# Optimization experiments

Measured on AMD Instinct MI355X. Metric: run time of the kernel, lower is better.

The kernel has to match this reference:

```python
import jax, jax.numpy as jnp
import numpy as np

N = 50000      # nodes
E = 400000     # edges per relation
R = 3          # edge types
D = 128        # input_dim == hidden_dim
H = 8          # attention heads
Dh = D // H    # per-head dim (16)
OUT = 1        # output logits
NEG_SLOPE = 0.2
LN_EPS = 1e-5


def setup_inputs() -> dict:
    key = jax.random.key(0)
    ks = jax.random.split(key, 20)
    s = 0.05
    f32 = jnp.float32
    return {
        "feat": jax.random.normal(ks[0], (N, D), f32),
        "edge_src": jax.random.randint(ks[1], (R, E), 0, N, dtype=jnp.int32),
        "edge_dst": jax.random.randint(ks[2], (R, E), 0, N, dtype=jnp.int32),
        # conv1: per-relation GATConv params (W, attn_l, attn_r, bias)
        "W1": jax.random.normal(ks[3], (R, D, H * Dh), f32) * s,
        "al1": jax.random.normal(ks[4], (R, H, Dh), f32) * s,
        "ar1": jax.random.normal(ks[5], (R, H, Dh), f32) * s,
        "b1": jnp.zeros((R, H * Dh), f32),
        # conv2
        "W2": jax.random.normal(ks[6], (R, D, H * Dh), f32) * s,
        "al2": jax.random.normal(ks[7], (R, H, Dh), f32) * s,
        "ar2": jax.random.normal(ks[8], (R, H, Dh), f32) * s,
        "b2": jnp.zeros((R, H * Dh), f32),
        # LayerNorm
        "ln_g": jnp.ones((D,), f32),
        "ln_b": jnp.zeros((D,), f32),
        # classifier MLP (dropout inactive at eval)
        "Wc1": jax.random.normal(ks[9], (D, D), f32) * s,
        "bc1": jnp.zeros((D,), f32),
        "Wc2": jax.random.normal(ks[10], (D, OUT), f32) * s,
        "bc2": jnp.zeros((OUT,), f32),
    }


def _gat(x, src, dst, W, al, ar, b):
    """DGL GATConv on one relation: x [N,Din] -> [N, H*Dh]."""
    h = (x @ W).reshape(N, H, Dh)                       # projected feats
    el = (h * al).sum(-1)                               # [N,H] src attn term
    er = (h * ar).sum(-1)                               # [N,H] dst attn term
    e = jax.nn.leaky_relu(el[src] + er[dst], NEG_SLOPE)  # [E,H]
    # edge-softmax over incoming edges per dst node, per head
    m = jax.ops.segment_max(e, dst, num_segments=N)     # [N,H]
    ex = jnp.exp(e - m[dst])
    denom = jax.ops.segment_sum(ex, dst, num_segments=N)
    alpha = ex / denom[dst]                             # [E,H]
    msg = alpha[:, :, None] * h[src]                    # [E,H,Dh]
    out = jax.ops.segment_sum(msg, dst, num_segments=N)  # [N,H,Dh]
    return out.reshape(N, H * Dh) + b


def _hetero(x, edge_src, edge_dst, W, al, ar, b):
    out = jnp.zeros((N, H * Dh), x.dtype)
    for r in range(R):  # small fixed relation count
        out = out + _gat(x, edge_src[r], edge_dst[r], W[r], al[r], ar[r], b[r])
    return out


def reference(feat, edge_src, edge_dst, W1, al1, ar1, b1, W2, al2, ar2, b2,
              ln_g, ln_b, Wc1, bc1, Wc2, bc2):
    h1 = jax.nn.relu(_hetero(feat, edge_src, edge_dst, W1, al1, ar1, b1))
    h2 = _hetero(h1, edge_src, edge_dst, W2, al2, ar2, b2)
    h = h2 + h1
    mu = h.mean(-1, keepdims=True)
    var = ((h - mu) ** 2).mean(-1, keepdims=True)
    h = (h - mu) * jax.lax.rsqrt(var + LN_EPS) * ln_g + ln_b
    h = jax.nn.relu(h @ Wc1 + bc1)
    return h @ Wc2 + bc2
```

## Files before the change

### kernel.cpp

```cpp
#include <hip/hip_runtime.h>
#include <math.h>

#define NN 50000
#define NE 400000
#define NREL 3
#define NCH 196

typedef __bf16 bf16x8 __attribute__((ext_vector_type(8)));
typedef float floatx4 __attribute__((ext_vector_type(4)));

__device__ __forceinline__ unsigned short f2bf(float f) {
  unsigned int u = __float_as_uint(f);
  return (unsigned short)((u + 0x7fffu + ((u >> 16) & 1u)) >> 16);
}

__global__ __launch_bounds__(256) void prep_wt(
    const float* __restrict__ W1, const float* __restrict__ W2,
    const float* __restrict__ Wc1, unsigned short* __restrict__ Wt) {
  int mat = blockIdx.x >> 3, slab = blockIdx.x & 7;
  const float* Wsrc = mat < 3 ? W1 + mat * 16384
                    : (mat < 6 ? W2 + (mat - 3) * 16384 : Wc1);
  unsigned short* dst = Wt + (size_t)mat * 144 * 128;
  int k0 = slab * 16;
#pragma unroll
  for (int i = 0; i < 8; ++i) {
    int idx = i * 256 + threadIdx.x;
    int k = k0 + (idx >> 7), nn = idx & 127;
    dst[nn * 128 + k] = f2bf(Wsrc[k * 128 + nn]);
  }
}

__global__ __launch_bounds__(256) void prep_attn(
    const float* __restrict__ W1, const float* __restrict__ W2,
    const float* __restrict__ al1, const float* __restrict__ ar1,
    const float* __restrict__ al2, const float* __restrict__ ar2,
    unsigned short* __restrict__ Wt) {
  int mat = blockIdx.x;
  const float* Wsrc = mat < 3 ? W1 + mat * 16384 : W2 + (mat - 3) * 16384;
  const float* alp = mat < 3 ? al1 + mat * 128 : al2 + (mat - 3) * 128;
  const float* arp = mat < 3 ? ar1 + mat * 128 : ar2 + (mat - 3) * 128;
  unsigned short* dst = Wt + (size_t)mat * 144 * 128;
#pragma unroll
  for (int i = 0; i < 8; ++i) {
    int j = i * 256 + threadIdx.x;
    int half = j >> 10, jj = j & 1023;
    int k = jj >> 3, h = jj & 7;
    const float* av = half ? arp : alp;
    float s = 0.f;
#pragma unroll
    for (int d = 0; d < 16; ++d) s += Wsrc[k * 128 + h * 16 + d] * av[h * 16 + d];
    dst[(128 + half * 8 + h) * 128 + k] = f2bf(s);
  }
}

__global__ __launch_bounds__(256) void gemm3_attn_mfma(
    const float* __restrict__ X, const unsigned short* __restrict__ Wt,
    unsigned short* __restrict__ hp, float* __restrict__ el,
    float* __restrict__ er, int n) {
  __shared__ unsigned short Xs[64 * 136];
  __shared__ unsigned short Ws[144 * 136];
  int t = threadIdx.x;
  int rowbase = blockIdx.x * 64;

  const float4* X4 = (const float4*)X;
#pragma unroll
  for (int i = 0; i < 8; ++i) {
    int v = t + i * 256;
    int row = v >> 5, k4 = (v & 31) * 4;
    float4 x = make_float4(0.f, 0.f, 0.f, 0.f);
    if (rowbase + row < n) x = X4[(size_t)(rowbase + row) * 32 + (v & 31)];
    ushort4 p;
    p.x = f2bf(x.x); p.y = f2bf(x.y); p.z = f2bf(x.z); p.w = f2bf(x.w);
    *(ushort4*)&Xs[row * 136 + k4] = p;
  }

  int lane = t & 63, wave = t >> 6;
  int quad = lane >> 4, l = lane & 15;

  for (int r = 0; r < NREL; ++r) {
    __syncthreads();
    const uint4* WtR = (const uint4*)(Wt + (size_t)r * 144 * 128);
#pragma unroll
    for (int i = 0; i < 9; ++i) {
      int v = t + i * 256;
      ((uint4*)Ws)[(v >> 4) * 17 + (v & 15)] = WtR[v];
    }
    __syncthreads();

    floatx4 acc[9];
#pragma unroll
    for (int i = 0; i < 9; ++i) acc[i] = floatx4{0.f, 0.f, 0.f, 0.f};
#pragma unroll
    for (int ks = 0; ks < 4; ++ks) {
      bf16x8 a = *(const bf16x8*)&Xs[(wave * 16 + l) * 136 + ks * 32 + quad * 8];
#pragma unroll
      for (int nt = 0; nt < 9; ++nt) {
        bf16x8 b = *(const bf16x8*)&Ws[(nt * 16 + l) * 136 + ks * 32 + quad * 8];
        acc[nt] = __builtin_amdgcn_mfma_f32_16x16x32_bf16(a, b, acc[nt], 0, 0, 0);
      }
    }

    unsigned short* hpR = hp + (size_t)r * NN * 128;
    float* elR = el + (size_t)r * NN * 8;
    float* erR = er + (size_t)r * NN * 8;
    int r0 = rowbase + wave * 16 + quad * 4;
#pragma unroll
    for (int reg = 0; reg < 4; ++reg) {
      int row = r0 + reg;
      if (row < n) {
#pragma unroll
        for (int nt = 0; nt < 8; ++nt)
          hpR[(size_t)row * 128 + nt * 16 + l] = f2bf(acc[nt][reg]);
        if (l < 8) elR[row * 8 + l] = acc[8][reg];
        else       erR[row * 8 + (l - 8)] = acc[8][reg];
      }
    }
  }
}

__global__ __launch_bounds__(256) void gemm_head_mfma(
    const float* __restrict__ X, const unsigned short* __restrict__ Wt,
    const float* __restrict__ bc1, const float* __restrict__ wc2,
    const float* __restrict__ bc2, float* __restrict__ out, int n) {
  __shared__ unsigned short Xs[64 * 136];
  __shared__ unsigned short Ws[128 * 136];
  int t = threadIdx.x;
  int rowbase = blockIdx.x * 64;

  const float4* X4 = (const float4*)X;
#pragma unroll
  for (int i = 0; i < 8; ++i) {
    int v = t + i * 256;
    int row = v >> 5, k4 = (v & 31) * 4;
    float4 x = make_float4(0.f, 0.f, 0.f, 0.f);
    if (rowbase + row < n) x = X4[(size_t)(rowbase + row) * 32 + (v & 31)];
    ushort4 p;
    p.x = f2bf(x.x); p.y = f2bf(x.y); p.z = f2bf(x.z); p.w = f2bf(x.w);
    *(ushort4*)&Xs[row * 136 + k4] = p;
  }
  const uint4* WtR = (const uint4*)Wt;
#pragma unroll
  for (int i = 0; i < 8; ++i) {
    int v = t + i * 256;
    ((uint4*)Ws)[(v >> 4) * 17 + (v & 15)] = WtR[v];
  }
  __syncthreads();

  int lane = t & 63, wave = t >> 6;
  int quad = lane >> 4, l = lane & 15;

  floatx4 acc[8];
#pragma unroll
  for (int i = 0; i < 8; ++i) acc[i] = floatx4{0.f, 0.f, 0.f, 0.f};
#pragma unroll
  for (int ks = 0; ks < 4; ++ks) {
    bf16x8 a = *(const bf16x8*)&Xs[(wave * 16 + l) * 136 + ks * 32 + quad * 8];
#pragma unroll
    for (int nt = 0; nt < 8; ++nt) {
      bf16x8 b = *(const bf16x8*)&Ws[(nt * 16 + l) * 136 + ks * 32 + quad * 8];
      acc[nt] = __builtin_amdgcn_mfma_f32_16x16x32_bf16(a, b, acc[nt], 0, 0, 0);
    }
  }

  float bv[8], wv[8];
#pragma unroll
  for (int nt = 0; nt < 8; ++nt) {
    bv[nt] = bc1[nt * 16 + l];
    wv[nt] = wc2[nt * 16 + l];
  }
  int r0 = rowbase + wave * 16 + quad * 4;
#pragma unroll
  for (int reg = 0; reg < 4; ++reg) {
    float s = 0.f;
#pragma unroll
    for (int nt = 0; nt < 8; ++nt)
      s += fmaxf(acc[nt][reg] + bv[nt], 0.f) * wv[nt];
    s += __shfl_xor(s, 1); s += __shfl_xor(s, 2);
    s += __shfl_xor(s, 4); s += __shfl_xor(s, 8);
    int row = r0 + reg;
    if (l == 0 && row < n) out[row] = s + bc2[0];
  }
}

__global__ __launch_bounds__(256) void hist_kernel(
    const int* __restrict__ edst, int* __restrict__ cnt, int* __restrict__ rank) {
  int t = blockIdx.x * 256 + threadIdx.x;
  if (t >= NREL * NE) return;
  int r = t / NE;
  rank[t] = atomicAdd(&cnt[r * NN + edst[t]], 1);
}

__global__ __launch_bounds__(256) void scan1(
    const int* __restrict__ cnt, int* __restrict__ partials) {
  __shared__ int s[256];
  int r = blockIdx.x / NCH, c = blockIdx.x % NCH;
  int i = c * 256 + threadIdx.x;
  s[threadIdx.x] = (i < NN) ? cnt[r * NN + i] : 0;
  __syncthreads();
  for (int off = 128; off; off >>= 1) {
    if (threadIdx.x < off) s[threadIdx.x] += s[threadIdx.x + off];
    __syncthreads();
  }
  if (threadIdx.x == 0) partials[r * NCH + c] = s[0];
}

__global__ __launch_bounds__(256) void scan2(int* __restrict__ partials) {
  __shared__ int s[256];
  int r = blockIdx.x;
  int t = threadIdx.x;
  int v = (t < NCH) ? partials[r * NCH + t] : 0;
  s[t] = v;
  __syncthreads();
  for (int off = 1; off < 256; off <<= 1) {
    int x = (t >= off) ? s[t - off] : 0;
    __syncthreads();
    s[t] += x;
    __syncthreads();
  }
  if (t < NCH) partials[r * NCH + t] = s[t] - v;
}

__global__ __launch_bounds__(256) void scan3(
    const int* __restrict__ cnt, const int* __restrict__ partials,
    int* __restrict__ rowptr) {
  __shared__ int s[256];
  int r = blockIdx.x / NCH, c = blockIdx.x % NCH;
  int t = threadIdx.x;
  int i = c * 256 + t;
  int v = (i < NN) ? cnt[r * NN + i] : 0;
  s[t] = v;
  __syncthreads();
  for (int off = 1; off < 256; off <<= 1) {
    int x = (t >= off) ? s[t - off] : 0;
    __syncthreads();
    s[t] += x;
    __syncthreads();
  }
  int base = partials[r * NCH + c];
  if (i < NN) rowptr[r * (NN + 1) + i] = base + s[t] - v;
  if (c == NCH - 1 && t == 0) rowptr[r * (NN + 1) + NN] = NE;
}

__global__ __launch_bounds__(256) void scatter_kernel(
    const int* __restrict__ esrc, const int* __restrict__ edst,
    const int* __restrict__ rowptr, const int* __restrict__ rank,
    int* __restrict__ col) {
  int t = blockIdx.x * 256 + threadIdx.x;
  if (t >= NREL * NE) return;
  int r = t / NE;
  int pos = rowptr[r * (NN + 1) + edst[t]] + rank[t];
  col[(size_t)r * NE + pos] = esrc[t];
}

__global__ __launch_bounds__(256) void gather_all(
    const int* __restrict__ rowptr, const int* __restrict__ col,
    const float* __restrict__ el, const float* __restrict__ er,
    const unsigned short* __restrict__ hp, const float* __restrict__ b,
    float* __restrict__ h1, const float* __restrict__ g,
    const float* __restrict__ beta, int mode) {
  int wid = (blockIdx.x * 256 + threadIdx.x) >> 6;
  int lane = threadIdx.x & 63;
  if (wid >= NN) return;
  int h = lane >> 3;
  int eoff = lane & 7;
  int c = lane * 2;

  int st3[NREL], en3[NREL], cv3[NREL];
  float er3[NREL];
#pragma unroll
  for (int r = 0; r < NREL; ++r) {
    const int* rp = rowptr + r * (NN + 1);
    st3[r] = rp[wid];
    en3[r] = rp[wid + 1];
    er3[r] = er[(size_t)r * NN * 8 + wid * 8 + h];
  }
#pragma unroll
  for (int r = 0; r < NREL; ++r) {
    int last = en3[r] - 1;
    last = last < st3[r] ? st3[r] : last;
    int i0 = st3[r] + eoff;
    cv3[r] = col[r * NE + (i0 < last ? i0 : last)];
  }

  float ax = 0.f, ay = 0.f;
#pragma unroll
  for (int r = 0; r < NREL; ++r) {
    int start = st3[r], end = en3[r];
    if (end > start) {
      const int* cl = col + r * NE;
      const float* elr = el + (size_t)r * NN * 8;
      const unsigned short* hpr = hp + (size_t)r * NN * 128;
      float er_me = er3[r];
      int last = end - 1;
      int idx = start + eoff;
      int colv = cv3[r];
      float den = 0.f, sx = 0.f, sy = 0.f;
      for (int i = start; i < end; i += 8) {
        int nidx = idx + 8;
        int colm = cl[nidx < last ? nidx : last];
        float e = elr[colv * 8 + h] + er_me;
        e = fmaxf(e, 0.2f * e);
        float x = (idx < end) ? __expf(e) : 0.f;
        den += x;
        unsigned int xi = __float_as_uint(x);
#define GATHER_EDGE(JJ)                                                        \
        {                                                                      \
          int sj = __builtin_amdgcn_readlane(colv, JJ);                        \
          const unsigned int* rowp = (const unsigned int*)(hpr + (size_t)sj * 128); \
          unsigned int u = rowp[lane];                                         \
          float xe = __uint_as_float(                                          \
              __builtin_amdgcn_ds_swizzle(xi, ((JJ) << 5) | 0x18));            \
          sx += xe * __uint_as_float(u << 16);                                 \
          sy += xe * __uint_as_float(u & 0xffff0000u);                         \
        }
        GATHER_EDGE(0)
        GATHER_EDGE(1)
        GATHER_EDGE(2)
        GATHER_EDGE(3)
        GATHER_EDGE(4)
        GATHER_EDGE(5)
        GATHER_EDGE(6)
        GATHER_EDGE(7)
#undef GATHER_EDGE
        idx = nidx;
        colv = colm;
      }
      den += __shfl_xor(den, 1);
      den += __shfl_xor(den, 2);
      den += __shfl_xor(den, 4);
      float inv = 1.f / den;
      ax += sx * inv;
      ay += sy * inv;
    }
  }

  float bx = b[c] + b[128 + c] + b[256 + c];
  float by = b[c + 1] + b[128 + c + 1] + b[256 + c + 1];
  float2* hptr = (float2*)&h1[(size_t)wid * 128 + c];
  if (mode == 0) {
    *hptr = make_float2(fmaxf(ax + bx, 0.f), fmaxf(ay + by, 0.f));
  } else {
    float2 r1 = *hptr;
    float vx = ax + bx + r1.x;
    float vy = ay + by + r1.y;
    float s = vx + vy;
#pragma unroll
    for (int off = 32; off; off >>= 1) s += __shfl_xor(s, off);
    float mu = s * (1.f / 128.f);
    float dx = vx - mu, dy = vy - mu;
    float sq = dx * dx + dy * dy;
#pragma unroll
    for (int off = 32; off; off >>= 1) sq += __shfl_xor(sq, off);
    float rstd = rsqrtf(sq * (1.f / 128.f) + 1e-5f);
    *hptr = make_float2(dx * rstd * g[c] + beta[c],
                        dy * rstd * g[c + 1] + beta[c + 1]);
  }
}

extern "C" void kernel_launch(void* const* d_in, const int* in_sizes, int n_in,
                              void* d_out, int out_size, void* d_ws, size_t ws_size,
                              hipStream_t stream) {
  const float* feat = (const float*)d_in[0];
  const int* esrc = (const int*)d_in[1];
  const int* edst = (const int*)d_in[2];
  const float* W1 = (const float*)d_in[3];
  const float* al1 = (const float*)d_in[4];
  const float* ar1 = (const float*)d_in[5];
  const float* b1 = (const float*)d_in[6];
  const float* W2 = (const float*)d_in[7];
  const float* al2 = (const float*)d_in[8];
  const float* ar2 = (const float*)d_in[9];
  const float* b2 = (const float*)d_in[10];
  const float* lng = (const float*)d_in[11];
  const float* lnb = (const float*)d_in[12];
  const float* Wc1 = (const float*)d_in[13];
  const float* bc1 = (const float*)d_in[14];
  const float* Wc2 = (const float*)d_in[15];
  const float* bc2 = (const float*)d_in[16];
  float* out = (float*)d_out;

  unsigned short* hp = (unsigned short*)d_ws;
  float* el = (float*)(hp + (size_t)3 * NN * 128);
  float* er = el + (size_t)3 * NN * 8;
  float* h1 = er + (size_t)3 * NN * 8;
  int* rowptr = (int*)(h1 + (size_t)NN * 128);
  int* col = rowptr + NREL * (NN + 1);
  int* cnt = col + (size_t)NREL * NE;
  int* partials = cnt + NREL * NN;
  unsigned short* Wt = (unsigned short*)(((uintptr_t)(partials + NREL * NCH) + 15)
                                         & ~(uintptr_t)15);
  int* rank = (int*)el;

  const int gemm_grid = (NN + 63) / 64;
  const int edge_grid = (NREL * NE + 255) / 256;
  const int gg_grid = (NN * 64) / 256;

  prep_wt<<<56, 256, 0, stream>>>(W1, W2, Wc1, Wt);
  prep_attn<<<6, 256, 0, stream>>>(W1, W2, al1, ar1, al2, ar2, Wt);

  (void)hipMemsetAsync(cnt, 0, (size_t)NREL * NN * sizeof(int), stream);
  hist_kernel<<<edge_grid, 256, 0, stream>>>(edst, cnt, rank);
  scan1<<<NREL * NCH, 256, 0, stream>>>(cnt, partials);
  scan2<<<NREL, 256, 0, stream>>>(partials);
  scan3<<<NREL * NCH, 256, 0, stream>>>(cnt, partials, rowptr);
  scatter_kernel<<<edge_grid, 256, 0, stream>>>(esrc, edst, rowptr, rank, col);

  gemm3_attn_mfma<<<gemm_grid, 256, 0, stream>>>(feat, Wt, hp, el, er, NN);
  gather_all<<<gg_grid, 256, 0, stream>>>(rowptr, col, el, er, hp, b1,
                                          h1, nullptr, nullptr, 0);
  gemm3_attn_mfma<<<gemm_grid, 256, 0, stream>>>(
      h1, Wt + (size_t)3 * 144 * 128, hp, el, er, NN);
  gather_all<<<gg_grid, 256, 0, stream>>>(rowptr, col, el, er, hp, b2,
                                          h1, lng, lnb, 1);
  gemm_head_mfma<<<gemm_grid, 256, 0, stream>>>(
      h1, Wt + (size_t)6 * 144 * 128, bc1, Wc2, bc2, out, NN);
}
```

Measured before the change: 372.3 us.

## Double GEMM row tile and read weight fragments directly from global

The per-relation GEMM now processes 128 rows per block, with each wave computing two 16-row M tiles. Each B fragment is loaded once and reused across both tiles. The weight matrix is no longer staged in shared memory; B fragments are read straight from global memory (L2/L1-cached), which removes two barriers per relation and the LDS copy. In exchange, register pressure roughly doubles with 18 accumulators, and the kernel depends on cache hits for the uncoalesced per-lane 16-byte weight loads.

After: 406.2 us. 9.1% more time.

```diff
diff --git a/kernel.cpp b/kernel.cpp
--- a/kernel.cpp
+++ b/kernel.cpp
@@ -57,14 +57,13 @@
     const float* __restrict__ X, const unsigned short* __restrict__ Wt,
     unsigned short* __restrict__ hp, float* __restrict__ el,
     float* __restrict__ er, int n) {
-  __shared__ unsigned short Xs[64 * 136];
-  __shared__ unsigned short Ws[144 * 136];
+  __shared__ unsigned short Xs[128 * 136];
   int t = threadIdx.x;
-  int rowbase = blockIdx.x * 64;
+  int rowbase = blockIdx.x * 128;
 
   const float4* X4 = (const float4*)X;
 #pragma unroll
-  for (int i = 0; i < 8; ++i) {
+  for (int i = 0; i < 16; ++i) {
     int v = t + i * 256;
     int row = v >> 5, k4 = (v & 31) * 4;
     float4 x = make_float4(0.f, 0.f, 0.f, 0.f);
@@ -73,46 +72,48 @@
     p.x = f2bf(x.x); p.y = f2bf(x.y); p.z = f2bf(x.z); p.w = f2bf(x.w);
     *(ushort4*)&Xs[row * 136 + k4] = p;
   }
+  __syncthreads();
 
   int lane = t & 63, wave = t >> 6;
   int quad = lane >> 4, l = lane & 15;
 
   for (int r = 0; r < NREL; ++r) {
-    __syncthreads();
-    const uint4* WtR = (const uint4*)(Wt + (size_t)r * 144 * 128);
-#pragma unroll
-    for (int i = 0; i < 9; ++i) {
-      int v = t + i * 256;
-      ((uint4*)Ws)[(v >> 4) * 17 + (v & 15)] = WtR[v];
-    }
-    __syncthreads();
-
-    floatx4 acc[9];
-#pragma unroll
-    for (int i = 0; i < 9; ++i) acc[i] = floatx4{0.f, 0.f, 0.f, 0.f};
+    const unsigned short* WtR = Wt + (size_t)r * 144 * 128;
+
+    floatx4 acc[2][9];
+#pragma unroll
+    for (int mt = 0; mt < 2; ++mt)
+#pragma unroll
+      for (int i = 0; i < 9; ++i) acc[mt][i] = floatx4{0.f, 0.f, 0.f, 0.f};
+
 #pragma unroll
     for (int ks = 0; ks < 4; ++ks) {
-      bf16x8 a = *(const bf16x8*)&Xs[(wave * 16 + l) * 136 + ks * 32 + quad * 8];
+      bf16x8 a0 = *(const bf16x8*)&Xs[(wave * 32 + l) * 136 + ks * 32 + quad * 8];
+      bf16x8 a1 = *(const bf16x8*)&Xs[(wave * 32 + 16 + l) * 136 + ks * 32 + quad * 8];
 #pragma unroll
       for (int nt = 0; nt < 9; ++nt) {
-        bf16x8 b = *(const bf16x8*)&Ws[(nt * 16 + l) * 136 + ks * 32 + quad * 8];
-        acc[nt] = __builtin_amdgcn_mfma_f32_16x16x32_bf16(a, b, acc[nt], 0, 0, 0);
+        bf16x8 b = *(const bf16x8*)&WtR[(size_t)(nt * 16 + l) * 128 + ks * 32 + quad * 8];
+        acc[0][nt] = __builtin_amdgcn_mfma_f32_16x16x32_bf16(a0, b, acc[0][nt], 0, 0, 0);
+        acc[1][nt] = __builtin_amdgcn_mfma_f32_16x16x32_bf16(a1, b, acc[1][nt], 0, 0, 0);
       }
     }
 
     unsigned short* hpR = hp + (size_t)r * NN * 128;
     float* elR = el + (size_t)r * NN * 8;
     float* erR = er + (size_t)r * NN * 8;
-    int r0 = rowbase + wave * 16 + quad * 4;
-#pragma unroll
-    for (int reg = 0; reg < 4; ++reg) {
-      int row = r0 + reg;
-      if (row < n) {
-#pragma unroll
-        for (int nt = 0; nt < 8; ++nt)
-          hpR[(size_t)row * 128 + nt * 16 + l] = f2bf(acc[nt][reg]);
-        if (l < 8) elR[row * 8 + l] = acc[8][reg];
-        else       erR[row * 8 + (l - 8)] = acc[8][reg];
+#pragma unroll
+    for (int mt = 0; mt < 2; ++mt) {
+      int r0 = rowbase + wave * 32 + mt * 16 + quad * 4;
+#pragma unroll
+      for (int reg = 0; reg < 4; ++reg) {
+        int row = r0 + reg;
+        if (row < n) {
+#pragma unroll
+          for (int nt = 0; nt < 8; ++nt)
+            hpR[(size_t)row * 128 + nt * 16 + l] = f2bf(acc[mt][nt][reg]);
+          if (l < 8) elR[row * 8 + l] = acc[mt][8][reg];
+          else       erR[row * 8 + (l - 8)] = acc[mt][8][reg];
+        }
       }
     }
   }
@@ -391,7 +392,8 @@
                                          & ~(uintptr_t)15);
   int* rank = (int*)el;
 
-  const int gemm_grid = (NN + 63) / 64;
+  const int gemm3_grid = (NN + 127) / 128;
+  const int head_grid = (NN + 63) / 64;
   const int edge_grid = (NREL * NE + 255) / 256;
   const int gg_grid = (NN * 64) / 256;
 
@@ -405,13 +407,13 @@
   scan3<<<NREL * NCH, 256, 0, stream>>>(cnt, partials, rowptr);
   scatter_kernel<<<edge_grid, 256, 0, stream>>>(esrc, edst, rowptr, rank, col);
 
-  gemm3_attn_mfma<<<gemm_grid, 256, 0, stream>>>(feat, Wt, hp, el, er, NN);
+  gemm3_attn_mfma<<<gemm3_grid, 256, 0, stream>>>(feat, Wt, hp, el, er, NN);
   gather_all<<<gg_grid, 256, 0, stream>>>(rowptr, col, el, er, hp, b1,
                                           h1, nullptr, nullptr, 0);
-  gemm3_attn_mfma<<<gemm_grid, 256, 0, stream>>>(
+  gemm3_attn_mfma<<<gemm3_grid, 256, 0, stream>>>(
       h1, Wt + (size_t)3 * 144 * 128, hp, el, er, NN);
   gather_all<<<gg_grid, 256, 0, stream>>>(rowptr, col, el, er, hp, b2,
                                           h1, lng, lnb, 1);
-  gemm_head_mfma<<<gemm_grid, 256, 0, stream>>>(
+  gemm_head_mfma<<<head_grid, 256, 0, stream>>>(
       h1, Wt + (size_t)6 * 144 * 128, bc1, Wc2, bc2, out, NN);
 }
```

## Load GEMM A-fragments directly to registers, parallelize prep, fold memset into prep

Applied to the files above, without the earlier changes.

The projection GEMM now loads each wave's X rows straight from global memory into bf16 MFMA A-fragments held in registers for all three relations. This removes the X shared-memory tile and one barrier, and adds a launch_bounds occupancy hint. The attention-vector prep kernel is spread over 48 blocks using float4 loads instead of 6 serial blocks. The count-buffer memset is folded into prep_wt to drop a separate launch. The direct per-lane X loads are less coalesced than the old cooperative tile load.

New measurement: 364.1 us. 1.02x faster.

```diff
diff --git a/kernel.cpp b/kernel.cpp
--- a/kernel.cpp
+++ b/kernel.cpp
@@ -16,7 +16,8 @@
 
 __global__ __launch_bounds__(256) void prep_wt(
     const float* __restrict__ W1, const float* __restrict__ W2,
-    const float* __restrict__ Wc1, unsigned short* __restrict__ Wt) {
+    const float* __restrict__ Wc1, unsigned short* __restrict__ Wt,
+    int* __restrict__ cnt) {
   int mat = blockIdx.x >> 3, slab = blockIdx.x & 7;
   const float* Wsrc = mat < 3 ? W1 + mat * 16384
                     : (mat < 6 ? W2 + (mat - 3) * 16384 : Wc1);
@@ -28,6 +29,8 @@
     int k = k0 + (idx >> 7), nn = idx & 127;
     dst[nn * 128 + k] = f2bf(Wsrc[k * 128 + nn]);
   }
+  for (int i = blockIdx.x * 256 + threadIdx.x; i < NREL * NN; i += 56 * 256)
+    cnt[i] = 0;
 }
 
 __global__ __launch_bounds__(256) void prep_attn(
@@ -35,50 +38,56 @@
     const float* __restrict__ al1, const float* __restrict__ ar1,
     const float* __restrict__ al2, const float* __restrict__ ar2,
     unsigned short* __restrict__ Wt) {
-  int mat = blockIdx.x;
+  int blk = blockIdx.x;
+  int mat = blk >> 3;
+  int half = (blk >> 2) & 1;
+  int kslab = blk & 3;
   const float* Wsrc = mat < 3 ? W1 + mat * 16384 : W2 + (mat - 3) * 16384;
-  const float* alp = mat < 3 ? al1 + mat * 128 : al2 + (mat - 3) * 128;
-  const float* arp = mat < 3 ? ar1 + mat * 128 : ar2 + (mat - 3) * 128;
-  unsigned short* dst = Wt + (size_t)mat * 144 * 128;
-#pragma unroll
-  for (int i = 0; i < 8; ++i) {
-    int j = i * 256 + threadIdx.x;
-    int half = j >> 10, jj = j & 1023;
-    int k = jj >> 3, h = jj & 7;
-    const float* av = half ? arp : alp;
-    float s = 0.f;
-#pragma unroll
-    for (int d = 0; d < 16; ++d) s += Wsrc[k * 128 + h * 16 + d] * av[h * 16 + d];
-    dst[(128 + half * 8 + h) * 128 + k] = f2bf(s);
-  }
-}
-
-__global__ __launch_bounds__(256) void gemm3_attn_mfma(
+  const float* av = half ? (mat < 3 ? ar1 + mat * 128 : ar2 + (mat - 3) * 128)
+                         : (mat < 3 ? al1 + mat * 128 : al2 + (mat - 3) * 128);
+  int h = threadIdx.x & 7;
+  int k = kslab * 32 + (threadIdx.x >> 3);
+  float s = 0.f;
+#pragma unroll
+  for (int j = 0; j < 4; ++j) {
+    float4 w = *(const float4*)&Wsrc[k * 128 + h * 16 + j * 4];
+    float4 a = *(const float4*)&av[h * 16 + j * 4];
+    s += w.x * a.x + w.y * a.y + w.z * a.z + w.w * a.w;
+  }
+  Wt[(size_t)mat * 144 * 128 + (128 + half * 8 + h) * 128 + k] = f2bf(s);
+}
+
+__global__ __launch_bounds__(256, 4) void gemm3_attn_mfma(
     const float* __restrict__ X, const unsigned short* __restrict__ Wt,
     unsigned short* __restrict__ hp, float* __restrict__ el,
     float* __restrict__ er, int n) {
-  __shared__ unsigned short Xs[64 * 136];
   __shared__ unsigned short Ws[144 * 136];
   int t = threadIdx.x;
-  int rowbase = blockIdx.x * 64;
-
-  const float4* X4 = (const float4*)X;
-#pragma unroll
-  for (int i = 0; i < 8; ++i) {
-    int v = t + i * 256;
-    int row = v >> 5, k4 = (v & 31) * 4;
-    float4 x = make_float4(0.f, 0.f, 0.f, 0.f);
-    if (rowbase + row < n) x = X4[(size_t)(rowbase + row) * 32 + (v & 31)];
-    ushort4 p;
-    p.x = f2bf(x.x); p.y = f2bf(x.y); p.z = f2bf(x.z); p.w = f2bf(x.w);
-    *(ushort4*)&Xs[row * 136 + k4] = p;
-  }
-
   int lane = t & 63, wave = t >> 6;
   int quad = lane >> 4, l = lane & 15;
+  int rowbase = blockIdx.x * 64;
+  int myrow = rowbase + wave * 16 + l;
+
+  bf16x8 afr[4];
+  const float4* X4 = (const float4*)X;
+#pragma unroll
+  for (int ks = 0; ks < 4; ++ks) {
+    float4 x0 = make_float4(0.f, 0.f, 0.f, 0.f), x1 = x0;
+    if (myrow < n) {
+      size_t base = (size_t)myrow * 32 + ks * 8 + quad * 2;
+      x0 = X4[base];
+      x1 = X4[base + 1];
+    }
+    union { unsigned short u[8]; bf16x8 v; } cv;
+    cv.u[0] = f2bf(x0.x); cv.u[1] = f2bf(x0.y);
+    cv.u[2] = f2bf(x0.z); cv.u[3] = f2bf(x0.w);
+    cv.u[4] = f2bf(x1.x); cv.u[5] = f2bf(x1.y);
+    cv.u[6] = f2bf(x1.z); cv.u[7] = f2bf(x1.w);
+    afr[ks] = cv.v;
+  }
 
   for (int r = 0; r < NREL; ++r) {
-    __syncthreads();
+    if (r > 0) __syncthreads();
     const uint4* WtR = (const uint4*)(Wt + (size_t)r * 144 * 128);
 #pragma unroll
     for (int i = 0; i < 9; ++i) {
@@ -92,11 +101,10 @@
     for (int i = 0; i < 9; ++i) acc[i] = floatx4{0.f, 0.f, 0.f, 0.f};
 #pragma unroll
     for (int ks = 0; ks < 4; ++ks) {
-      bf16x8 a = *(const bf16x8*)&Xs[(wave * 16 + l) * 136 + ks * 32 + quad * 8];
 #pragma unroll
       for (int nt = 0; nt < 9; ++nt) {
         bf16x8 b = *(const bf16x8*)&Ws[(nt * 16 + l) * 136 + ks * 32 + quad * 8];
-        acc[nt] = __builtin_amdgcn_mfma_f32_16x16x32_bf16(a, b, acc[nt], 0, 0, 0);
+        acc[nt] = __builtin_amdgcn_mfma_f32_16x16x32_bf16(afr[ks], b, acc[nt], 0, 0, 0);
       }
     }
 
@@ -391,27 +399,27 @@
                                          & ~(uintptr_t)15);
   int* rank = (int*)el;
 
-  const int gemm_grid = (NN + 63) / 64;
+  const int gemm3_grid = (NN + 63) / 64;
+  const int head_grid = (NN + 63) / 64;
   const int edge_grid = (NREL * NE + 255) / 256;
   const int gg_grid = (NN * 64) / 256;
 
-  prep_wt<<<56, 256, 0, stream>>>(W1, W2, Wc1, Wt);
-  prep_attn<<<6, 256, 0, stream>>>(W1, W2, al1, ar1, al2, ar2, Wt);
-
-  (void)hipMemsetAsync(cnt, 0, (size_t)NREL * NN * sizeof(int), stream);
+  prep_wt<<<56, 256, 0, stream>>>(W1, W2, Wc1, Wt, cnt);
+  prep_attn<<<48, 256, 0, stream>>>(W1, W2, al1, ar1, al2, ar2, Wt);
+
   hist_kernel<<<edge_grid, 256, 0, stream>>>(edst, cnt, rank);
   scan1<<<NREL * NCH, 256, 0, stream>>>(cnt, partials);
   scan2<<<NREL, 256, 0, stream>>>(partials);
   scan3<<<NREL * NCH, 256, 0, stream>>>(cnt, partials, rowptr);
   scatter_kernel<<<edge_grid, 256, 0, stream>>>(esrc, edst, rowptr, rank, col);
 
-  gemm3_attn_mfma<<<gemm_grid, 256, 0, stream>>>(feat, Wt, hp, el, er, NN);
+  gemm3_attn_mfma<<<gemm3_grid, 256, 0, stream>>>(feat, Wt, hp, el, er, NN);
   gather_all<<<gg_grid, 256, 0, stream>>>(rowptr, col, el, er, hp, b1,
                                           h1, nullptr, nullptr, 0);
-  gemm3_attn_mfma<<<gemm_grid, 256, 0, stream>>>(
+  gemm3_attn_mfma<<<gemm3_grid, 256, 0, stream>>>(
       h1, Wt + (size_t)3 * 144 * 128, hp, el, er, NN);
   gather_all<<<gg_grid, 256, 0, stream>>>(rowptr, col, el, er, hp, b2,
                                           h1, lng, lnb, 1);
-  gemm_head_mfma<<<gemm_grid, 256, 0, stream>>>(
+  gemm_head_mfma<<<head_grid, 256, 0, stream>>>(
       h1, Wt + (size_t)6 * 144 * 128, bc1, Wc2, bc2, out, NN);
 }
```
